# Kernel tuning notes

Measured on AMD Instinct MI355X. Metric: run time of the kernel, lower is better.

The kernel has to match this reference:

```python
import jax, jax.numpy as jnp
import numpy as np

N = 128            # number of delay lines
BUFFER_LEN = 48000 # delay buffer length (samples)
SCALE = 1.0
N_BINS = 64        # reflection filter taps


def setup_inputs() -> dict:
    key = jax.random.key(0)
    k1, k2, k3, k4 = jax.random.split(key, 4)
    return {
        "buffer": jax.random.normal(k1, (N, BUFFER_LEN), dtype=jnp.float32),
        "inputs": jax.random.normal(k2, (N,), dtype=jnp.float32),
        # fractional delays in samples, in [0, 32)
        "delays": jax.random.uniform(k3, (N,), dtype=jnp.float32) * 32.0,
        "reflection_filters": jax.random.normal(k4, (N, N_BINS), dtype=jnp.float32),
    }


def reference(buffer, inputs, delays, reflection_filters):
    K = 2 * BUFFER_LEN
    # FIFO push: roll left, write newest sample at the end
    buf = jnp.roll(buffer, -1, axis=-1).at[:, -1].set(inputs)
    # zero-pad to FFT length K
    buffer_pad = jnp.pad(buf, ((0, 0), (0, K - BUFFER_LEN)))
    fft_buffer = jnp.fft.fft(buffer_pad, axis=-1)  # [N, K] complex

    d = SCALE * delays[:, None]  # [N, 1]
    two_pi_over_K = 2.0 * jnp.pi / K
    omega_left = two_pi_over_K * jnp.arange(K // 2, dtype=jnp.float32)[None, :]          # [1, K/2]
    omega_right = two_pi_over_K * (K - jnp.arange(K // 2 + 1, K, dtype=jnp.float32))[None, :]  # [1, K/2-1]

    # Pei-Lai closed-form fractional delay filter
    H_left = jnp.exp(-1j * (omega_left * d))                 # [N, K/2]
    H_mid = jnp.cos(jnp.pi * d).astype(jnp.complex64)        # [N, 1] (Nyquist bin)
    H_right = jnp.exp(1j * (omega_right * d))                # [N, K/2-1]
    H = jnp.concatenate([H_left, H_mid, H_right], axis=1)    # [N, K]

    delayed = jnp.fft.ifft(H * fft_buffer, axis=-1).real.astype(jnp.float32)  # [N, K]

    # weighted slice of the n_bins taps preceding the read head
    taps = delayed[:, BUFFER_LEN - N_BINS - 1 : BUFFER_LEN - 1]  # [N, n_bins]
    outputs = (reflection_filters * taps).sum(-1)                # [N]
    return outputs[:, None]                                      # [N, 1]
```

## Files before the change

### kernel.cpp

```cpp
#include <hip/hip_runtime.h>
#include <hip/hip_bf16.h>
#include <math.h>

#define NLINES 128
#define BUFLEN 48000
#define KLEN   96000
#define NBINS  64
#define TAP1   47936
#define PSLOW  47840
#define NG8    5980
#define NFULL  5
#define NREST  860
#define NTHR   1024
#define NW     16
#define NTK    10

#define INV2K  5.2083333333333333e-06f
#define DLT_F  3.2724923474893679e-05f
#define T05    1.6362461737446e-05f
#define T15    4.9087385252705e-05f
#define T25    8.1812308687e-05f
#define T35    1.1453723216e-04f

__device__ __forceinline__ float wave_reduce(float v){
  #pragma unroll
  for (int off = 32; off; off >>= 1) v += __shfl_down(v, off, 64);
  return v;
}

__device__ __forceinline__ float sin_pi_d(float d){
  const float r = rintf(d);
  float sp = __builtin_amdgcn_sinf(0.5f * (d - r));
  if (((int)r) & 1) sp = -sp;
  return sp;
}

__global__ __launch_bounds__(NTHR) void frac_delay_line(
    const float* __restrict__ buffer, const float* __restrict__ inputs,
    const float* __restrict__ delays, const float* __restrict__ filt,
    float* __restrict__ out)
{
  const int line = blockIdx.x;
  const int tid  = threadIdx.x;
  const int lane = tid & 63, wv = tid >> 6;

  __shared__ float redM[NW][5];
  __shared__ float redT[NW][NBINS];

  const float d = delays[line];
  const float scale0 = sin_pi_d(d) * (1.0f / (float)KLEN);
  const float* __restrict__ bufline = buffer + (size_t)line * BUFLEN;

  const float cb = 47964.0f - d;
  float A0=0.f, A1=0.f, A2=0.f, A3=0.f, A4=0.f;

  auto moment8 = [&](int P, float4 va, float4 vb){
    const float tr = (cb - (float)P) * INV2K;
    const float s  = __builtin_amdgcn_sinf(tr);
    const float c  = __builtin_amdgcn_cosf(tr);
    const float TBL[8] = {T35, T25, T15, T05, -T05, -T15, -T25, -T35};
    const float vv[8]  = {va.x, va.y, va.z, va.w, vb.x, vb.y, vb.z, vb.w};
    float N[8], D[8], Pp[8], w[8];
    #pragma unroll
    for (int i = 0; i < 8; ++i){
      N[i] = fmaf(s, -TBL[i], c);
      D[i] = fmaf(c,  TBL[i], s);
    }
    Pp[0] = D[0];
    #pragma unroll
    for (int i = 1; i < 8; ++i) Pp[i] = Pp[i-1] * D[i];
    float inv = __builtin_amdgcn_rcpf(Pp[7]);
    #pragma unroll
    for (int i = 7; i >= 1; --i){ w[i] = N[i] * (inv * Pp[i-1]); inv *= D[i]; }
    w[0] = N[0] * inv;
    #pragma unroll
    for (int i = 0; i < 8; ++i){
      const float vp = (i & 1) ? -vv[i] : vv[i];
      const float W  = w[i];
      const float w2 = W * W;
      const float u  = w2 + 1.0f;
      A0 = fmaf(vp, W, A0);
      const float vu = vp * u;
      A1 += vu;
      const float t2 = vu * W;
      A2 += t2;
      const float e3 = fmaf(3.0f, w2, 1.0f);
      A3 = fmaf(vu, e3, A3);
      A4 = fmaf(t2, e3 + 1.0f, A4);
    }
  };

  {
    int P = tid << 3;
    float4 va = *reinterpret_cast<const float4*>(bufline + P);
    float4 vb = *reinterpret_cast<const float4*>(bufline + P + 4);
    if (tid == 0) va.x = 0.f;
    #pragma unroll
    for (int k = 0; k < NFULL; ++k){
      int Pn = 0; float4 na, nb;
      const bool more = (k < NFULL - 1) || (tid < NREST);
      if (more){
        Pn = (k < NFULL - 1) ? ((tid + (k + 1) * NTHR) << 3)
                             : ((NFULL * NTHR + tid) << 3);
        na = *reinterpret_cast<const float4*>(bufline + Pn);
        nb = *reinterpret_cast<const float4*>(bufline + Pn + 4);
      }
      moment8(P, va, vb);
      P = Pn; va = na; vb = nb;
    }
    if (tid < NREST) moment8(P, va, vb);
  }

  const int j  = lane;
  const int jj = TAP1 + j;
  float tj = 0.f;
  #pragma unroll
  for (int k = 0; k < NTK; ++k){
    const int p = PSLOW + wv + (k << 4);
    const float v = bufline[p];
    const float x = (float)(jj - p) - d;
    float term;
    if (x == 0.0f) term = v;
    else {
      const float tr = x * INV2K;
      const float ct = __builtin_amdgcn_cosf(tr) *
                       __builtin_amdgcn_rcpf(__builtin_amdgcn_sinf(tr));
      const float sg = ((j + p) & 1) ? 1.0f : -1.0f;
      term = sg * scale0 * v * ct;
    }
    tj += term;
  }
  if (wv == 0){
    const float v = inputs[line];
    const int   p = BUFLEN;
    const float x = (float)(jj - p) - d;
    const float tr = x * INV2K;
    const float ct = __builtin_amdgcn_cosf(tr) *
                     __builtin_amdgcn_rcpf(__builtin_amdgcn_sinf(tr));
    const float sg = ((j + p) & 1) ? 1.0f : -1.0f;
    tj += sg * scale0 * v * ct;
  }

  float vals[5] = {A0, A1, A2, A3, A4};
  #pragma unroll
  for (int k = 0; k < 5; ++k){
    float x = wave_reduce(vals[k]);
    if (lane == 0) redM[wv][k] = x;
  }
  redT[wv][j] = tj;
  __syncthreads();

  if (wv == 0){
    float mom[5];
    #pragma unroll
    for (int k = 0; k < 5; ++k){
      float s = 0.f;
      #pragma unroll
      for (int w = 0; w < NW; ++w) s += redM[w][k];
      mom[k] = s;
    }
    float tail = 0.f;
    #pragma unroll
    for (int w = 0; w < NW; ++w) tail += redT[w][lane];

    const float Y = ((float)lane - 31.5f) * DLT_F;
    float h =          mom[4] * (1.0f/3.0f);
    h = fmaf(h, Y,    -mom[3] * (1.0f/3.0f));
    h = fmaf(h, Y,     mom[2]);
    h = fmaf(h, Y,    -mom[1]);
    h = fmaf(h, Y,     mom[0]);
    const float sg = (lane & 1) ? 1.0f : -1.0f;
    const float tap = fmaf(sg * scale0, h, tail);
    float val = tap * filt[line * NBINS + lane];
    val = wave_reduce(val);
    if (lane == 0) out[line] = val;
  }
}

extern "C" void kernel_launch(void* const* d_in, const int* in_sizes, int n_in,
                              void* d_out, int out_size, void* d_ws, size_t ws_size,
                              hipStream_t stream)
{
  const float* buffer = (const float*)d_in[0];
  const float* inputs = (const float*)d_in[1];
  const float* delays = (const float*)d_in[2];
  const float* filt   = (const float*)d_in[3];
  float* out = (float*)d_out;

  frac_delay_line<<<NLINES, NTHR, 0, stream>>>(buffer, inputs, delays, filt, out);
}
```

Baseline: 15.18 us.

## Split each delay line across two blocks and combine partial sums

Each line's moment accumulation is split between two blocks (256 blocks instead of 128) to fill more of the GPU's compute units. One block handles the first three chunks and the other handles the rest plus the tail taps. Each block writes a partial filtered output to workspace, and a second tiny kernel adds the pairs. This costs an extra kernel launch and a workspace round trip, and the two halves are unevenly loaded.

Result: faster. 14.21 us (-6.4%).

```diff
diff --git a/kernel.cpp b/kernel.cpp
--- a/kernel.cpp
+++ b/kernel.cpp
@@ -9,7 +9,7 @@
 #define TAP1   47936
 #define PSLOW  47840
 #define NG8    5980
-#define NFULL  5
+#define G1     3072
 #define NREST  860
 #define NTHR   1024
 #define NW     16
@@ -35,12 +35,13 @@
   return sp;
 }
 
-__global__ __launch_bounds__(NTHR) void frac_delay_line(
+__global__ __launch_bounds__(NTHR) void frac_delay_part(
     const float* __restrict__ buffer, const float* __restrict__ inputs,
     const float* __restrict__ delays, const float* __restrict__ filt,
-    float* __restrict__ out)
+    float* __restrict__ ws)
 {
-  const int line = blockIdx.x;
+  const int line = blockIdx.x >> 1;
+  const int role = blockIdx.x & 1;
   const int tid  = threadIdx.x;
   const int lane = tid & 63, wv = tid >> 6;
 
@@ -90,55 +91,71 @@
     }
   };
 
-  {
+  if (role == 0){
     int P = tid << 3;
     float4 va = *reinterpret_cast<const float4*>(bufline + P);
     float4 vb = *reinterpret_cast<const float4*>(bufline + P + 4);
     if (tid == 0) va.x = 0.f;
     #pragma unroll
-    for (int k = 0; k < NFULL; ++k){
+    for (int k = 0; k < 3; ++k){
       int Pn = 0; float4 na, nb;
-      const bool more = (k < NFULL - 1) || (tid < NREST);
-      if (more){
-        Pn = (k < NFULL - 1) ? ((tid + (k + 1) * NTHR) << 3)
-                             : ((NFULL * NTHR + tid) << 3);
+      if (k < 2){
+        Pn = (tid + (k + 1) * NTHR) << 3;
         na = *reinterpret_cast<const float4*>(bufline + Pn);
         nb = *reinterpret_cast<const float4*>(bufline + Pn + 4);
       }
       moment8(P, va, vb);
       P = Pn; va = na; vb = nb;
     }
+  } else {
+    int P = (G1 + tid) << 3;
+    float4 va = *reinterpret_cast<const float4*>(bufline + P);
+    float4 vb = *reinterpret_cast<const float4*>(bufline + P + 4);
+    #pragma unroll
+    for (int k = 0; k < 2; ++k){
+      int Pn = 0; float4 na, nb;
+      const bool more = (k < 1) || (tid < NREST);
+      if (more){
+        Pn = (G1 + (k + 1) * NTHR + tid) << 3;
+        na = *reinterpret_cast<const float4*>(bufline + Pn);
+        nb = *reinterpret_cast<const float4*>(bufline + Pn + 4);
+      }
+      moment8(P, va, vb);
+      P = Pn; va = na; vb = nb;
+    }
     if (tid < NREST) moment8(P, va, vb);
   }
 
-  const int j  = lane;
-  const int jj = TAP1 + j;
   float tj = 0.f;
-  #pragma unroll
-  for (int k = 0; k < NTK; ++k){
-    const int p = PSLOW + wv + (k << 4);
-    const float v = bufline[p];
-    const float x = (float)(jj - p) - d;
-    float term;
-    if (x == 0.0f) term = v;
-    else {
+  if (role == 1){
+    const int j  = lane;
+    const int jj = TAP1 + j;
+    #pragma unroll
+    for (int k = 0; k < NTK; ++k){
+      const int p = PSLOW + wv + (k << 4);
+      const float v = bufline[p];
+      const float x = (float)(jj - p) - d;
+      float term;
+      if (x == 0.0f) term = v;
+      else {
+        const float tr = x * INV2K;
+        const float ct = __builtin_amdgcn_cosf(tr) *
+                         __builtin_amdgcn_rcpf(__builtin_amdgcn_sinf(tr));
+        const float sg = ((j + p) & 1) ? 1.0f : -1.0f;
+        term = sg * scale0 * v * ct;
+      }
+      tj += term;
+    }
+    if (wv == 0){
+      const float v = inputs[line];
+      const int   p = BUFLEN;
+      const float x = (float)(jj - p) - d;
       const float tr = x * INV2K;
       const float ct = __builtin_amdgcn_cosf(tr) *
                        __builtin_amdgcn_rcpf(__builtin_amdgcn_sinf(tr));
       const float sg = ((j + p) & 1) ? 1.0f : -1.0f;
-      term = sg * scale0 * v * ct;
-    }
-    tj += term;
-  }
-  if (wv == 0){
-    const float v = inputs[line];
-    const int   p = BUFLEN;
-    const float x = (float)(jj - p) - d;
-    const float tr = x * INV2K;
-    const float ct = __builtin_amdgcn_cosf(tr) *
-                     __builtin_amdgcn_rcpf(__builtin_amdgcn_sinf(tr));
-    const float sg = ((j + p) & 1) ? 1.0f : -1.0f;
-    tj += sg * scale0 * v * ct;
+      tj += sg * scale0 * v * ct;
+    }
   }
 
   float vals[5] = {A0, A1, A2, A3, A4};
@@ -147,7 +164,7 @@
     float x = wave_reduce(vals[k]);
     if (lane == 0) redM[wv][k] = x;
   }
-  redT[wv][j] = tj;
+  redT[wv][lane] = tj;
   __syncthreads();
 
   if (wv == 0){
@@ -160,9 +177,10 @@
       mom[k] = s;
     }
     float tail = 0.f;
-    #pragma unroll
-    for (int w = 0; w < NW; ++w) tail += redT[w][lane];
-
+    if (role == 1){
+      #pragma unroll
+      for (int w = 0; w < NW; ++w) tail += redT[w][lane];
+    }
     const float Y = ((float)lane - 31.5f) * DLT_F;
     float h =          mom[4] * (1.0f/3.0f);
     h = fmaf(h, Y,    -mom[3] * (1.0f/3.0f));
@@ -173,8 +191,15 @@
     const float tap = fmaf(sg * scale0, h, tail);
     float val = tap * filt[line * NBINS + lane];
     val = wave_reduce(val);
-    if (lane == 0) out[line] = val;
-  }
+    if (lane == 0) ws[blockIdx.x] = val;
+  }
+}
+
+__global__ __launch_bounds__(NLINES) void frac_delay_combine(
+    const float* __restrict__ ws, float* __restrict__ out)
+{
+  const int t = threadIdx.x;
+  out[t] = ws[2 * t] + ws[2 * t + 1];
 }
 
 extern "C" void kernel_launch(void* const* d_in, const int* in_sizes, int n_in,
@@ -186,6 +211,8 @@
   const float* delays = (const float*)d_in[2];
   const float* filt   = (const float*)d_in[3];
   float* out = (float*)d_out;
-
-  frac_delay_line<<<NLINES, NTHR, 0, stream>>>(buffer, inputs, delays, filt, out);
-}
+  float* ws  = (float*)d_ws;
+
+  frac_delay_part<<<2 * NLINES, NTHR, 0, stream>>>(buffer, inputs, delays, filt, ws);
+  frac_delay_combine<<<1, NLINES, 0, stream>>>(ws, out);
+}
```

## Split each delay line across four blocks and combine partials in second kernel

Applied to the files above, without the earlier changes.

Each line's moment accumulation is divided among four blocks (roles), giving 512 blocks instead of 128 so more of the GPU's compute units are busy. Partial outputs go to workspace and a small second kernel sums them. The per-group moment evaluation now uses 4-sample groups with one sin/cos pair each, which is a finer grain than the previous 8-sample groups. The extra kernel launch and the workspace round trip add fixed overhead, and role 3 carries both the tail taps and a share of the groups, so the load across roles is uneven.

After: 16.26 us. 7.1% more time.

```diff
diff --git a/kernel.cpp b/kernel.cpp
--- a/kernel.cpp
+++ b/kernel.cpp
@@ -9,18 +9,15 @@
 #define TAP1   47936
 #define PSLOW  47840
 #define NG8    5980
-#define NFULL  5
-#define NREST  860
 #define NTHR   1024
 #define NW     16
 #define NTK    10
+#define ROLES  4
 
 #define INV2K  5.2083333333333333e-06f
 #define DLT_F  3.2724923474893679e-05f
 #define T05    1.6362461737446e-05f
 #define T15    4.9087385252705e-05f
-#define T25    8.1812308687e-05f
-#define T35    1.1453723216e-04f
 
 __device__ __forceinline__ float wave_reduce(float v){
   #pragma unroll
@@ -35,12 +32,13 @@
   return sp;
 }
 
-__global__ __launch_bounds__(NTHR) void frac_delay_line(
+__global__ __launch_bounds__(NTHR, 8) void frac_delay_part(
     const float* __restrict__ buffer, const float* __restrict__ inputs,
     const float* __restrict__ delays, const float* __restrict__ filt,
-    float* __restrict__ out)
+    float* __restrict__ ws)
 {
-  const int line = blockIdx.x;
+  const int line = blockIdx.x >> 2;
+  const int role = blockIdx.x & 3;
   const int tid  = threadIdx.x;
   const int lane = tid & 63, wv = tid >> 6;
 
@@ -51,31 +49,29 @@
   const float scale0 = sin_pi_d(d) * (1.0f / (float)KLEN);
   const float* __restrict__ bufline = buffer + (size_t)line * BUFLEN;
 
-  const float cb = 47964.0f - d;
+  const float cb = 47966.0f - d;
   float A0=0.f, A1=0.f, A2=0.f, A3=0.f, A4=0.f;
 
-  auto moment8 = [&](int P, float4 va, float4 vb){
+  auto moment4 = [&](int P, float4 v){
     const float tr = (cb - (float)P) * INV2K;
     const float s  = __builtin_amdgcn_sinf(tr);
     const float c  = __builtin_amdgcn_cosf(tr);
-    const float TBL[8] = {T35, T25, T15, T05, -T05, -T15, -T25, -T35};
-    const float vv[8]  = {va.x, va.y, va.z, va.w, vb.x, vb.y, vb.z, vb.w};
-    float N[8], D[8], Pp[8], w[8];
+    const float D0 = fmaf(c,  T15, s), N0 = fmaf(s, -T15, c);
+    const float D1 = fmaf(c,  T05, s), N1 = fmaf(s, -T05, c);
+    const float D2 = fmaf(c, -T05, s), N2 = fmaf(s,  T05, c);
+    const float D3 = fmaf(c, -T15, s), N3 = fmaf(s,  T15, c);
+    const float P2 = D0*D1, P3 = P2*D2, P4 = P3*D3;
+    const float inv = __builtin_amdgcn_rcpf(P4);
+    const float I3 = inv*P3;
+    const float r1 = inv*D3;
+    const float I2 = r1*P2;
+    const float r2 = r1*D2;
+    const float I1 = r2*D0, I0 = r2*D1;
+    const float w[4] = {N0*I0, N1*I1, N2*I2, N3*I3};
+    const float vv[4] = {v.x, -v.y, v.z, -v.w};
     #pragma unroll
-    for (int i = 0; i < 8; ++i){
-      N[i] = fmaf(s, -TBL[i], c);
-      D[i] = fmaf(c,  TBL[i], s);
-    }
-    Pp[0] = D[0];
-    #pragma unroll
-    for (int i = 1; i < 8; ++i) Pp[i] = Pp[i-1] * D[i];
-    float inv = __builtin_amdgcn_rcpf(Pp[7]);
-    #pragma unroll
-    for (int i = 7; i >= 1; --i){ w[i] = N[i] * (inv * Pp[i-1]); inv *= D[i]; }
-    w[0] = N[0] * inv;
-    #pragma unroll
-    for (int i = 0; i < 8; ++i){
-      const float vp = (i & 1) ? -vv[i] : vv[i];
+    for (int i = 0; i < 4; ++i){
+      const float vp = vv[i];
       const float W  = w[i];
       const float w2 = W * W;
       const float u  = w2 + 1.0f;
@@ -90,55 +86,53 @@
     }
   };
 
-  {
-    int P = tid << 3;
+  auto do_group = [&](int g){
+    const int P = g << 3;
     float4 va = *reinterpret_cast<const float4*>(bufline + P);
     float4 vb = *reinterpret_cast<const float4*>(bufline + P + 4);
-    if (tid == 0) va.x = 0.f;
+    if (P == 0) va.x = 0.f;
+    moment4(P, va);
+    moment4(P + 4, vb);
+  };
+
+  float tj = 0.f;
+  if (role == 0){
+    do_group(tid); do_group(1024 + tid);
+  } else if (role == 1){
+    do_group(2048 + tid); do_group(3072 + tid);
+  } else if (role == 2){
+    do_group(4096 + tid);
+    if (tid < 560) do_group(5120 + tid);
+  } else {
+    if (tid < 300) do_group(5680 + tid);
+    const int j  = lane;
+    const int jj = TAP1 + j;
     #pragma unroll
-    for (int k = 0; k < NFULL; ++k){
-      int Pn = 0; float4 na, nb;
-      const bool more = (k < NFULL - 1) || (tid < NREST);
-      if (more){
-        Pn = (k < NFULL - 1) ? ((tid + (k + 1) * NTHR) << 3)
-                             : ((NFULL * NTHR + tid) << 3);
-        na = *reinterpret_cast<const float4*>(bufline + Pn);
-        nb = *reinterpret_cast<const float4*>(bufline + Pn + 4);
+    for (int k = 0; k < NTK; ++k){
+      const int p = PSLOW + wv + (k << 4);
+      const float v = bufline[p];
+      const float x = (float)(jj - p) - d;
+      float term;
+      if (x == 0.0f) term = v;
+      else {
+        const float tr = x * INV2K;
+        const float ct = __builtin_amdgcn_cosf(tr) *
+                         __builtin_amdgcn_rcpf(__builtin_amdgcn_sinf(tr));
+        const float sg = ((j + p) & 1) ? 1.0f : -1.0f;
+        term = sg * scale0 * v * ct;
       }
-      moment8(P, va, vb);
-      P = Pn; va = na; vb = nb;
+      tj += term;
     }
-    if (tid < NREST) moment8(P, va, vb);
-  }
-
-  const int j  = lane;
-  const int jj = TAP1 + j;
-  float tj = 0.f;
-  #pragma unroll
-  for (int k = 0; k < NTK; ++k){
-    const int p = PSLOW + wv + (k << 4);
-    const float v = bufline[p];
-    const float x = (float)(jj - p) - d;
-    float term;
-    if (x == 0.0f) term = v;
-    else {
+    if (wv == 0){
+      const float v = inputs[line];
+      const int   p = BUFLEN;
+      const float x = (float)(jj - p) - d;
       const float tr = x * INV2K;
       const float ct = __builtin_amdgcn_cosf(tr) *
                        __builtin_amdgcn_rcpf(__builtin_amdgcn_sinf(tr));
       const float sg = ((j + p) & 1) ? 1.0f : -1.0f;
-      term = sg * scale0 * v * ct;
+      tj += sg * scale0 * v * ct;
     }
-    tj += term;
-  }
-  if (wv == 0){
-    const float v = inputs[line];
-    const int   p = BUFLEN;
-    const float x = (float)(jj - p) - d;
-    const float tr = x * INV2K;
-    const float ct = __builtin_amdgcn_cosf(tr) *
-                     __builtin_amdgcn_rcpf(__builtin_amdgcn_sinf(tr));
-    const float sg = ((j + p) & 1) ? 1.0f : -1.0f;
-    tj += sg * scale0 * v * ct;
   }
 
   float vals[5] = {A0, A1, A2, A3, A4};
@@ -147,7 +141,7 @@
     float x = wave_reduce(vals[k]);
     if (lane == 0) redM[wv][k] = x;
   }
-  redT[wv][j] = tj;
+  redT[wv][lane] = tj;
   __syncthreads();
 
   if (wv == 0){
@@ -160,9 +154,10 @@
       mom[k] = s;
     }
     float tail = 0.f;
-    #pragma unroll
-    for (int w = 0; w < NW; ++w) tail += redT[w][lane];
-
+    if (role == 3){
+      #pragma unroll
+      for (int w = 0; w < NW; ++w) tail += redT[w][lane];
+    }
     const float Y = ((float)lane - 31.5f) * DLT_F;
     float h =          mom[4] * (1.0f/3.0f);
     h = fmaf(h, Y,    -mom[3] * (1.0f/3.0f));
@@ -173,8 +168,15 @@
     const float tap = fmaf(sg * scale0, h, tail);
     float val = tap * filt[line * NBINS + lane];
     val = wave_reduce(val);
-    if (lane == 0) out[line] = val;
+    if (lane == 0) ws[blockIdx.x] = val;
   }
+}
+
+__global__ __launch_bounds__(NLINES) void frac_delay_combine(
+    const float* __restrict__ ws, float* __restrict__ out)
+{
+  const int t = threadIdx.x;
+  out[t] = (ws[4*t] + ws[4*t+1]) + (ws[4*t+2] + ws[4*t+3]);
 }
 
 extern "C" void kernel_launch(void* const* d_in, const int* in_sizes, int n_in,
@@ -186,6 +188,8 @@
   const float* delays = (const float*)d_in[2];
   const float* filt   = (const float*)d_in[3];
   float* out = (float*)d_out;
+  float* ws  = (float*)d_ws;
 
-  frac_delay_line<<<NLINES, NTHR, 0, stream>>>(buffer, inputs, delays, filt, out);
+  frac_delay_part<<<ROLES * NLINES, NTHR, 0, stream>>>(buffer, inputs, delays, filt, ws);
+  frac_delay_combine<<<1, NLINES, 0, stream>>>(ws, out);
 }
```
